# Performance work log

Measured on AMD Instinct MI355X. Metric: run time of the kernel, lower is better.

The kernel has to match this reference:

```python
import jax, jax.numpy as jnp
import numpy as np

B, S, D = 32, 4096, 64          # batch, max seq len, input_dim
P, STRIDE, H = 8, 4, 512        # patch_size, patch_stride, hidden_size
T = (S - P) // STRIDE + 1       # static max token count (sample 0 has length S)
EPS = 1e-6


def setup_inputs() -> dict:
    key = jax.random.key(0)
    k1, k2, k3 = jax.random.split(key, 3)
    x = jax.random.normal(k1, (B, S, D), dtype=jnp.float32)
    lengths = jax.random.randint(k2, (B,), P, S + 1)
    lengths = lengths.at[0].set(S)  # at least one full-length sample -> max_tokens == T
    W = jax.random.normal(k3, (P * D, H), dtype=jnp.float32) / np.sqrt(P * D)
    b = jnp.zeros((H,), dtype=jnp.float32)
    scale = jnp.ones((H,), dtype=jnp.float32)  # RMSNorm scale
    return {"x": x, "lengths": lengths, "W": W, "b": b, "scale": scale}


def _patch(x, lengths):
    # number of tokens per sample: len(range(0, max(L-P+1, 1), STRIDE))
    n_tok = jnp.where(lengths >= P, (lengths - P) // STRIDE + 1, 1)  # [B]
    # gather positions for every (token, within-patch) slot
    pos = jnp.arange(T)[:, None] * STRIDE + jnp.arange(P)[None, :]   # [T, P]
    tokens = x[:, pos, :]                                            # [B, T, P, D]
    valid = (pos[None, :, :] < lengths[:, None, None]) \
          & (jnp.arange(T)[None, :, None] < n_tok[:, None, None])    # [B, T, P]
    tokens = jnp.where(valid[..., None], tokens, 0.0)
    return tokens.reshape(B, T, P * D), n_tok


def reference(x, lengths, W, b, scale):
    tokens, token_lengths = _patch(x, lengths)        # [B, T, P*D], [B]
    h = tokens @ W + b                                # proj -> [B, T, H]
    rms = jnp.sqrt(jnp.mean(h * h, axis=-1, keepdims=True) + EPS)
    hidden = h / rms * scale                          # RMSNorm
    return hidden, token_lengths, tokens
```

## Files before the change

### kernel.cpp

```cpp
#include <hip/hip_runtime.h>
#include <hip/hip_bf16.h>

constexpr int Bc = 32, Sc = 4096, Dc = 64, Pc = 8, STRIDEc = 4, Hc = 512;
constexpr int Tc = (Sc - Pc) / STRIDEc + 1;
constexpr int Kc = Pc * Dc;
constexpr float EPSc = 1e-6f;
constexpr int PITCH = 40;

typedef __bf16 bf16x8 __attribute__((ext_vector_type(8)));
typedef unsigned short ushort8 __attribute__((ext_vector_type(8)));
typedef float f32x4 __attribute__((ext_vector_type(4)));

__device__ __forceinline__ int n_tok_of(int len) {
    return (len >= Pc) ? ((len - Pc) / STRIDEc + 1) : 1;
}

__device__ __forceinline__ unsigned short f2bf(float f) {
    unsigned u = __builtin_bit_cast(unsigned, f);
    u = (u + 0x7FFFu + ((u >> 16) & 1u)) >> 16;
    return (unsigned short)u;
}

__global__ __launch_bounds__(256) void prep_kernel(
        const float* __restrict__ W, const int* __restrict__ lengths,
        unsigned short* __restrict__ Wt, float* __restrict__ out_tl) {
    __shared__ float tile[32][33];
    const int k0 = blockIdx.x * 32, n0 = blockIdx.y * 32;
    const int r = threadIdx.x >> 3, c = (threadIdx.x & 7) * 4;
    const float4 v = *(const float4*)(W + (size_t)(k0 + r) * Hc + n0 + c);
    tile[c + 0][r] = v.x;
    tile[c + 1][r] = v.y;
    tile[c + 2][r] = v.z;
    tile[c + 3][r] = v.w;
    __syncthreads();
    ushort4 o;
    o.x = f2bf(tile[r][c + 0]);
    o.y = f2bf(tile[r][c + 1]);
    o.z = f2bf(tile[r][c + 2]);
    o.w = f2bf(tile[r][c + 3]);
    *(ushort4*)(Wt + (size_t)blockIdx.x * (Hc * 32) + (size_t)(n0 + r) * 32 + c) = o;
    if (blockIdx.x == 0 && blockIdx.y == 0 && threadIdx.x < Bc)
        out_tl[threadIdx.x] = (float)n_tok_of(lengths[threadIdx.x]);
}

__global__ __launch_bounds__(256, 2) void fused_kernel(
        const float* __restrict__ x, const int* __restrict__ lengths,
        const unsigned short* __restrict__ Wt, const float* __restrict__ bias,
        const float* __restrict__ scale, float* __restrict__ hidden,
        float* __restrict__ tokens) {
    const int b  = blockIdx.y;
    const int t0 = blockIdx.x * 64;
    const int len = lengths[b];
    const int ntok = n_tok_of(len);
    const int tid = threadIdx.x;

    float* tokb = tokens + (size_t)b * Tc * Kc;

    if (t0 >= ntok) {
        __shared__ float red[4];
        const int w = tid >> 6, lane = tid & 63;
        const float2 b2 = *(const float2*)(bias + tid * 2);
        float s = b2.x * b2.x + b2.y * b2.y;
#pragma unroll
        for (int off = 32; off; off >>= 1) s += __shfl_xor(s, off);
        if (lane == 0) red[w] = s;
        __syncthreads();
        const float rstd = rsqrtf((red[0] + red[1] + red[2] + red[3])
                                  * (1.0f / (float)Hc) + EPSc);
        const int c4 = (tid & 127) * 4;
        const f32x4 cvec = *(const f32x4*)(bias + c4) * rstd
                         * *(const f32x4*)(scale + c4);
        const f32x4 z = {0.f, 0.f, 0.f, 0.f};
        float* hidb = hidden + ((size_t)b * Tc + t0) * Hc;
        float* tokp = tokb + (size_t)t0 * Kc;
        const int r0 = tid >> 7;
#pragma unroll 8
        for (int rr = r0; rr < 64; rr += 2) {
            if (t0 + rr < Tc) {
                __builtin_nontemporal_store(cvec, (f32x4*)(hidb + (size_t)rr * Hc + c4));
                __builtin_nontemporal_store(z,    (f32x4*)(tokp + (size_t)rr * Kc + c4));
            }
        }
        return;
    }

    __shared__ unsigned short As[2][64 * PITCH];
    __shared__ float ssbuf[4][64];

    const int w    = tid >> 6;
    const int lane = tid & 63;
    const int l15  = lane & 15;
    const int quad = lane >> 4;

    f32x4 acc[4][8];
#pragma unroll
    for (int tt = 0; tt < 4; ++tt)
#pragma unroll
        for (int ct = 0; ct < 8; ++ct) acc[tt][ct] = (f32x4){0.f, 0.f, 0.f, 0.f};

    const float* xb = x + (size_t)b * (Sc * Dc);

    int a_r[2], a_c[2];  bool a_tv[2], a_lv[2];  const float* a_src[2];
#pragma unroll
    for (int it = 0; it < 2; ++it) {
        const int l = tid + it * 256;
        a_r[it] = l >> 3;
        a_c[it] = (l & 7) * 4;
        const int t = t0 + a_r[it];
        a_tv[it] = (t < Tc);
        a_lv[it] = (t < ntok);
        a_src[it] = xb + (size_t)t * (STRIDEc * Dc);
    }

    f32x4   ra[2];
    ushort8 rbA[8], rbB[8];

    const unsigned short* wfrag = Wt + ((w * 128 + l15) * 32 + quad * 8);

#pragma unroll
    for (int it = 0; it < 2; ++it) {
        ra[it] = (f32x4){0.f, 0.f, 0.f, 0.f};
        if (a_lv[it]) ra[it] = *(const f32x4*)(a_src[it] + a_c[it]);
    }
#pragma unroll
    for (int ct = 0; ct < 8; ++ct)
        rbA[ct] = *(const ushort8*)(wfrag + ct * 512);

    auto do_step = [&](const int step, ushort8 (&rbC)[8], ushort8 (&rbN)[8]) {
        const int p  = step & 1;
        const int k0 = step * 32;
#pragma unroll
        for (int it = 0; it < 2; ++it) {
            const f32x4 v = ra[it];
            if (a_tv[it])
                __builtin_nontemporal_store(v,
                    (f32x4*)(tokb + (size_t)(t0 + a_r[it]) * Kc + k0 + a_c[it]));
            ushort4 h4;
            h4.x = f2bf(v[0]); h4.y = f2bf(v[1]); h4.z = f2bf(v[2]); h4.w = f2bf(v[3]);
            *(ushort4*)(&As[p][0] + a_r[it] * PITCH + a_c[it]) = h4;
        }
        __syncthreads();
        bf16x8 btok[4];
#pragma unroll
        for (int tt = 0; tt < 4; ++tt)
            btok[tt] = __builtin_bit_cast(bf16x8,
                *(const ushort8*)(&As[p][0] + (tt * 16 + l15) * PITCH + quad * 8));
        if (step < 15) {
            const int kn = k0 + 32;
#pragma unroll
            for (int it = 0; it < 2; ++it) {
                ra[it] = (f32x4){0.f, 0.f, 0.f, 0.f};
                if (a_lv[it]) ra[it] = *(const f32x4*)(a_src[it] + kn + a_c[it]);
            }
            const unsigned short* wn = wfrag + (size_t)(step + 1) * (Hc * 32);
#pragma unroll
            for (int ct = 0; ct < 8; ++ct)
                rbN[ct] = *(const ushort8*)(wn + ct * 512);
        }
#pragma unroll
        for (int ct = 0; ct < 8; ++ct) {
            const bf16x8 aW = __builtin_bit_cast(bf16x8, rbC[ct]);
#pragma unroll
            for (int tt = 0; tt < 4; ++tt)
                acc[tt][ct] = __builtin_amdgcn_mfma_f32_16x16x32_bf16(
                    aW, btok[tt], acc[tt][ct], 0, 0, 0);
        }
    };

#pragma unroll
    for (int sp = 0; sp < 8; ++sp) {
        do_step(2 * sp,     rbA, rbB);
        do_step(2 * sp + 1, rbB, rbA);
    }

    float ss[4] = {0.f, 0.f, 0.f, 0.f};
#pragma unroll
    for (int ct = 0; ct < 8; ++ct) {
        const f32x4 b4 = *(const f32x4*)(bias + w * 128 + ct * 16 + quad * 4);
#pragma unroll
        for (int tt = 0; tt < 4; ++tt) {
            f32x4 h = acc[tt][ct] + b4;
            acc[tt][ct] = h;
            ss[tt] += h[0] * h[0] + h[1] * h[1] + h[2] * h[2] + h[3] * h[3];
        }
    }
#pragma unroll
    for (int tt = 0; tt < 4; ++tt) {
        float s = ss[tt];
        s += __shfl_xor(s, 16);
        s += __shfl_xor(s, 32);
        if (quad == 0) ssbuf[w][tt * 16 + l15] = s;
    }
    __syncthreads();
    float rstd[4];
#pragma unroll
    for (int tt = 0; tt < 4; ++tt) {
        const int r = tt * 16 + l15;
        const float tot = ssbuf[0][r] + ssbuf[1][r] + ssbuf[2][r] + ssbuf[3][r];
        rstd[tt] = rsqrtf(tot * (1.0f / (float)Hc) + EPSc);
    }
#pragma unroll
    for (int ct = 0; ct < 8; ++ct) {
        const f32x4 s4 = *(const f32x4*)(scale + w * 128 + ct * 16 + quad * 4);
#pragma unroll
        for (int tt = 0; tt < 4; ++tt) {
            const int t = t0 + tt * 16 + l15;
            if (t < Tc) {
                f32x4 o = acc[tt][ct] * rstd[tt] * s4;
                __builtin_nontemporal_store(o,
                    (f32x4*)(hidden + ((size_t)b * Tc + t) * Hc
                             + w * 128 + ct * 16 + quad * 4));
            }
        }
    }
}

extern "C" void kernel_launch(void* const* d_in, const int* in_sizes, int n_in,
                              void* d_out, int out_size, void* d_ws, size_t ws_size,
                              hipStream_t stream) {
    const float* x       = (const float*)d_in[0];
    const int*   lengths = (const int*)d_in[1];
    const float* W       = (const float*)d_in[2];
    const float* bias    = (const float*)d_in[3];
    const float* scale   = (const float*)d_in[4];

    const size_t BTH = (size_t)Bc * Tc * Hc;
    float* out    = (float*)d_out;
    float* hidden = out;
    float* tl     = out + BTH;
    float* tokens = out + BTH + Bc;

    unsigned short* Wt = (unsigned short*)d_ws;

    {
        dim3 grid(Hc / 32, Hc / 32);
        prep_kernel<<<grid, 256, 0, stream>>>(W, lengths, Wt, tl);
    }
    {
        dim3 grid(16, Bc);
        fused_kernel<<<grid, 256, 0, stream>>>(x, lengths, Wt, bias, scale,
                                               hidden, tokens);
    }
}
```

Measured before the change: 192.6 us.

## Stage whole 64x512 token tile in LDS upfront, drop per-step barriers

```diff
diff --git a/kernel.cpp b/kernel.cpp
--- a/kernel.cpp
+++ b/kernel.cpp
@@ -5,7 +5,7 @@
 constexpr int Tc = (Sc - Pc) / STRIDEc + 1;
 constexpr int Kc = Pc * Dc;
 constexpr float EPSc = 1e-6f;
-constexpr int PITCH = 40;
+constexpr int APITCH = 520;
 
 typedef __bf16 bf16x8 __attribute__((ext_vector_type(8)));
 typedef unsigned short ushort8 __attribute__((ext_vector_type(8)));
@@ -84,7 +84,7 @@
         return;
     }
 
-    __shared__ unsigned short As[2][64 * PITCH];
+    __shared__ unsigned short As[64 * APITCH];
     __shared__ float ssbuf[4][64];
 
     const int w    = tid >> 6;
@@ -92,66 +92,45 @@
     const int l15  = lane & 15;
     const int quad = lane >> 4;
 
-    f32x4 acc[4][8];
-#pragma unroll
-    for (int tt = 0; tt < 4; ++tt)
-#pragma unroll
-        for (int ct = 0; ct < 8; ++ct) acc[tt][ct] = (f32x4){0.f, 0.f, 0.f, 0.f};
-
     const float* xb = x + (size_t)b * (Sc * Dc);
 
-    int a_r[2], a_c[2];  bool a_tv[2], a_lv[2];  const float* a_src[2];
-#pragma unroll
-    for (int it = 0; it < 2; ++it) {
-        const int l = tid + it * 256;
-        a_r[it] = l >> 3;
-        a_c[it] = (l & 7) * 4;
-        const int t = t0 + a_r[it];
-        a_tv[it] = (t < Tc);
-        a_lv[it] = (t < ntok);
-        a_src[it] = xb + (size_t)t * (STRIDEc * Dc);
-    }
-
-    f32x4   ra[2];
+    const unsigned short* wfrag = Wt + ((w * 128 + l15) * 32 + quad * 8);
+
     ushort8 rbA[8], rbB[8];
-
-    const unsigned short* wfrag = Wt + ((w * 128 + l15) * 32 + quad * 8);
-
-#pragma unroll
-    for (int it = 0; it < 2; ++it) {
-        ra[it] = (f32x4){0.f, 0.f, 0.f, 0.f};
-        if (a_lv[it]) ra[it] = *(const f32x4*)(a_src[it] + a_c[it]);
-    }
 #pragma unroll
     for (int ct = 0; ct < 8; ++ct)
         rbA[ct] = *(const ushort8*)(wfrag + ct * 512);
 
+#pragma unroll 8
+    for (int it = 0; it < 32; ++it) {
+        const int c   = tid + it * 256;
+        const int r   = c >> 7;
+        const int col = (c & 127) * 4;
+        const int t   = t0 + r;
+        f32x4 v = {0.f, 0.f, 0.f, 0.f};
+        if (t < ntok) v = *(const f32x4*)(xb + (size_t)t * (STRIDEc * Dc) + col);
+        if (t < Tc)
+            __builtin_nontemporal_store(v, (f32x4*)(tokb + (size_t)t * Kc + col));
+        ushort4 h4;
+        h4.x = f2bf(v[0]); h4.y = f2bf(v[1]); h4.z = f2bf(v[2]); h4.w = f2bf(v[3]);
+        *(ushort4*)(As + r * APITCH + col) = h4;
+    }
+    __syncthreads();
+
+    f32x4 acc[4][8];
+#pragma unroll
+    for (int tt = 0; tt < 4; ++tt)
+#pragma unroll
+        for (int ct = 0; ct < 8; ++ct) acc[tt][ct] = (f32x4){0.f, 0.f, 0.f, 0.f};
+
     auto do_step = [&](const int step, ushort8 (&rbC)[8], ushort8 (&rbN)[8]) {
-        const int p  = step & 1;
         const int k0 = step * 32;
-#pragma unroll
-        for (int it = 0; it < 2; ++it) {
-            const f32x4 v = ra[it];
-            if (a_tv[it])
-                __builtin_nontemporal_store(v,
-                    (f32x4*)(tokb + (size_t)(t0 + a_r[it]) * Kc + k0 + a_c[it]));
-            ushort4 h4;
-            h4.x = f2bf(v[0]); h4.y = f2bf(v[1]); h4.z = f2bf(v[2]); h4.w = f2bf(v[3]);
-            *(ushort4*)(&As[p][0] + a_r[it] * PITCH + a_c[it]) = h4;
-        }
-        __syncthreads();
         bf16x8 btok[4];
 #pragma unroll
         for (int tt = 0; tt < 4; ++tt)
             btok[tt] = __builtin_bit_cast(bf16x8,
-                *(const ushort8*)(&As[p][0] + (tt * 16 + l15) * PITCH + quad * 8));
+                *(const ushort8*)(As + (tt * 16 + l15) * APITCH + k0 + quad * 8));
         if (step < 15) {
-            const int kn = k0 + 32;
-#pragma unroll
-            for (int it = 0; it < 2; ++it) {
-                ra[it] = (f32x4){0.f, 0.f, 0.f, 0.f};
-                if (a_lv[it]) ra[it] = *(const f32x4*)(a_src[it] + kn + a_c[it]);
-            }
             const unsigned short* wn = wfrag + (size_t)(step + 1) * (Hc * 32);
 #pragma unroll
             for (int ct = 0; ct < 8; ++ct)
@@ -166,7 +145,6 @@
                     aW, btok[tt], acc[tt][ct], 0, 0, 0);
         }
     };
-
 #pragma unroll
     for (int sp = 0; sp < 8; ++sp) {
         do_step(2 * sp,     rbA, rbB);
```

Result: slower. 201.4 us (+4.5%).
